# Optimization experiments

Hardware: AMD Instinct MI355X
Metric: run time of the kernel (lower is better)

The kernel has to match this reference:

```python
import jax, jax.numpy as jnp
import numpy as np

N_NODES = 50000
N_EDGES = 600000
N_GRAPHS = 256
N_FL1, N_MPL, N_FL2, N_FL3 = 128, 128, 128, 64
EPS = 1e-12


def _glorot(key, shape):
    lim = float(np.sqrt(6.0 / (shape[0] + shape[1])))
    return jax.random.uniform(key, shape, jnp.float32, -lim, lim)


def setup_inputs() -> dict:
    key = jax.random.key(0)
    ks = jax.random.split(key, 16)
    x = jax.random.normal(ks[0], (N_NODES, 5), jnp.float32)
    edge_index = jax.random.randint(ks[1], (2, N_EDGES), 0, N_NODES, jnp.int64)
    batch = jnp.sort(jax.random.randint(ks[2], (N_NODES,), 0, N_GRAPHS, jnp.int64))
    return {
        "x": x,
        "edge_index": edge_index,
        "batch": batch,
        "W_pre": _glorot(ks[3], (5, N_FL1)),
        "b_pre": jnp.zeros((N_FL1,), jnp.float32),
        "W1_l": _glorot(ks[4], (N_FL1, N_MPL)),
        "b1": jnp.zeros((N_MPL,), jnp.float32),
        "W1_r": _glorot(ks[5], (N_FL1, N_MPL)),
        "W2_l": _glorot(ks[6], (N_MPL, N_MPL)),
        "b2": jnp.zeros((N_MPL,), jnp.float32),
        "W2_r": _glorot(ks[7], (N_MPL, N_MPL)),
        "W_p1": _glorot(ks[8], (N_MPL, N_FL2)),
        "b_p1": jnp.zeros((N_FL2,), jnp.float32),
        "W_p2": _glorot(ks[9], (N_FL2, N_FL3)),
        "b_p2": jnp.zeros((N_FL3,), jnp.float32),
        "W_out": _glorot(ks[10], (N_FL3, 1)),
        "b_out": jnp.zeros((1,), jnp.float32),
    }


def _sage_conv(x, src, dst, deg_inv, W_l, b_l, W_r):
    # mean-aggregate neighbor messages x[src] onto dst, then linear transforms
    agg = jax.ops.segment_sum(x[src], dst, num_segments=N_NODES) * deg_inv  # [N, d]
    out = agg @ W_l + b_l + x @ W_r
    # normalize=True -> L2 normalize per node (PyG F.normalize, eps=1e-12)
    norm = jnp.sqrt(jnp.sum(out * out, axis=-1, keepdims=True))
    return out / jnp.maximum(norm, EPS)


def reference(x, edge_index, batch, W_pre, b_pre, W1_l, b1, W1_r,
              W2_l, b2, W2_r, W_p1, b_p1, W_p2, b_p2, W_out, b_out):
    src, dst = edge_index[0], edge_index[1]
    deg = jax.ops.segment_sum(jnp.ones((N_EDGES,), jnp.float32), dst, num_segments=N_NODES)
    deg_inv = (1.0 / jnp.maximum(deg, 1.0))[:, None]

    h = jax.nn.relu(x @ W_pre + b_pre)
    h = jax.nn.relu(_sage_conv(h, src, dst, deg_inv, W1_l, b1, W1_r))
    h = jax.nn.relu(_sage_conv(h, src, dst, deg_inv, W2_l, b2, W2_r))

    # global_mean_pool over graph ids in batch
    g_sum = jax.ops.segment_sum(h, batch, num_segments=N_GRAPHS)  # [G, d]
    g_cnt = jax.ops.segment_sum(jnp.ones((N_NODES,), jnp.float32), batch, num_segments=N_GRAPHS)
    g = g_sum / jnp.maximum(g_cnt, 1.0)[:, None]

    g = jax.nn.relu(g @ W_p1 + b_p1)
    g = jax.nn.relu(g @ W_p2 + b_p2)
    return g @ W_out + b_out  # [G, 1]
```

## Files before the change

### kernel.cpp

```cpp
#include <hip/hip_runtime.h>
#include <hip/hip_bf16.h>

#define N_NODES 50000
#define N_EDGES 600000
#define N_GRAPHS 256
#define D 128
#define NTILES 1563

typedef __bf16 bf16x8 __attribute__((ext_vector_type(8)));
typedef float f32x16 __attribute__((ext_vector_type(16)));
typedef unsigned short u16x8 __attribute__((ext_vector_type(8)));
typedef unsigned short u16x4 __attribute__((ext_vector_type(4)));

__device__ __forceinline__ float bf2f(unsigned short u) {
    unsigned v = ((unsigned)u) << 16;
    return __builtin_bit_cast(float, v);
}
__device__ __forceinline__ unsigned short f2bf(float f) {
    unsigned x = __builtin_bit_cast(unsigned, f);
    unsigned r = (x + 0x7fffu + ((x >> 16) & 1u)) >> 16;
    return (unsigned short)r;
}


__global__ void zero_int_kernel(int* __restrict__ p, int n) {
    int i = blockIdx.x * 256 + threadIdx.x;
    if (i < n) p[i] = 0;
}

__global__ void deg_kernel(const int* __restrict__ dst, int* __restrict__ deg) {
    int e = blockIdx.x * 256 + threadIdx.x;
    if (e < N_EDGES) atomicAdd(&deg[dst[e]], 1);
}

__global__ __launch_bounds__(1024) void scan_blk_kernel(const int* __restrict__ deg,
                                                        int* __restrict__ partial,
                                                        int* __restrict__ bsum) {
    __shared__ int tmp[1024];
    int tid = threadIdx.x;
    int i = blockIdx.x * 1024 + tid;
    int v = (i < N_NODES) ? deg[i] : 0;
    tmp[tid] = v;
    __syncthreads();
    for (int off = 1; off < 1024; off <<= 1) {
        int add = (tid >= off) ? tmp[tid - off] : 0;
        __syncthreads();
        tmp[tid] += add;
        __syncthreads();
    }
    if (i < N_NODES) partial[i] = tmp[tid] - v;
    if (tid == 1023) bsum[blockIdx.x] = tmp[tid];
}

__global__ void scan_top_kernel(const int* __restrict__ bsum, int* __restrict__ boff,
                                int* __restrict__ row_start, int nblk) {
    int l = threadIdx.x;
    int v = (l < nblk) ? bsum[l] : 0;
    int incl = v;
#pragma unroll
    for (int m = 1; m < 64; m <<= 1) {
        int t = __shfl_up(incl, m);
        if (l >= m) incl += t;
    }
    if (l < nblk) boff[l] = incl - v;
    if (l == 63) row_start[N_NODES] = incl;
}

__global__ void scan_fix_kernel(const int* __restrict__ partial, const int* __restrict__ boff,
                                const int* __restrict__ deg, int* __restrict__ row_start,
                                int* __restrict__ cursor, float* __restrict__ deg_inv) {
    int i = blockIdx.x * 256 + threadIdx.x;
    if (i >= N_NODES) return;
    int rs = partial[i] + boff[i >> 10];
    row_start[i] = rs;
    cursor[i] = rs;
    deg_inv[i] = 1.0f / fmaxf((float)deg[i], 1.0f);
}

__global__ void fill_kernel(const int* __restrict__ src, const int* __restrict__ dst,
                            int* __restrict__ cursor, int* __restrict__ csr_src) {
    int e = blockIdx.x * 256 + threadIdx.x;
    if (e < N_EDGES) {
        int slot = atomicAdd(&cursor[dst[e]], 1);
        csr_src[slot] = src[e];
    }
}


__global__ void pack_w_kernel(const float* __restrict__ Wl1, const float* __restrict__ Wr1,
                              const float* __restrict__ Wl2, const float* __restrict__ Wr2,
                              unsigned short* __restrict__ Wp) {
    int tid = blockIdx.x * 256 + threadIdx.x;
    int conv = tid >> 15;
    int e = tid & 32767;
    int j = e & 7, lane = (e >> 3) & 63, ct = (e >> 9) & 3, kt = e >> 11;
    int k = kt * 16 + (lane >> 5) * 8 + j;
    int col = (lane & 31) * 4 + ct;
    const float* Wl = conv ? Wl2 : Wl1;
    const float* Wr = conv ? Wr2 : Wr1;
    float v = (k < 128) ? Wl[k * 128 + col] : Wr[(k - 128) * 128 + col];
    Wp[tid] = f2bf(v);
}


__global__ void pre_kernel(const float* __restrict__ x, const float* __restrict__ Wp,
                           const float* __restrict__ bp, unsigned short* __restrict__ h0) {
    int idx = blockIdx.x * 256 + threadIdx.x;
    if (idx >= N_NODES * 16) return;
    int node = idx >> 4, j8 = (idx & 15) * 8;
    const float* xr = x + node * 5;
    float acc[8];
#pragma unroll
    for (int c = 0; c < 8; ++c) acc[c] = bp[j8 + c];
#pragma unroll
    for (int k = 0; k < 5; ++k) {
        float xv = xr[k];
#pragma unroll
        for (int c = 0; c < 8; ++c) acc[c] += xv * Wp[k * D + j8 + c];
    }
    u16x8 o;
#pragma unroll
    for (int c = 0; c < 8; ++c) o[c] = f2bf(fmaxf(acc[c], 0.f));
    *(u16x8*)&h0[(size_t)node * D + j8] = o;
}


__global__ __launch_bounds__(256) void agg_kernel(const unsigned short* __restrict__ h,
                                                  const int* __restrict__ row_start,
                                                  const int* __restrict__ csr_src,
                                                  const float* __restrict__ deg_inv,
                                                  unsigned short* __restrict__ aggb) {
    int node = blockIdx.x * 16 + (threadIdx.x >> 4);
    int fl = threadIdx.x & 15;
    if (node >= N_NODES) return;
    int s = row_start[node], e = row_start[node + 1];
    float a[8] = {0.f, 0.f, 0.f, 0.f, 0.f, 0.f, 0.f, 0.f};
    int i = s;
    for (; i + 3 < e; i += 4) {
        int c0 = csr_src[i];
        int c1 = csr_src[i + 1];
        int c2 = csr_src[i + 2];
        int c3 = csr_src[i + 3];
        bf16x8 v0 = *(const bf16x8*)(h + (size_t)c0 * D + fl * 8);
        bf16x8 v1 = *(const bf16x8*)(h + (size_t)c1 * D + fl * 8);
        bf16x8 v2 = *(const bf16x8*)(h + (size_t)c2 * D + fl * 8);
        bf16x8 v3 = *(const bf16x8*)(h + (size_t)c3 * D + fl * 8);
#pragma unroll
        for (int j = 0; j < 8; ++j)
            a[j] += ((float)v0[j] + (float)v1[j]) + ((float)v2[j] + (float)v3[j]);
    }
    for (; i < e; ++i) {
        int c0 = csr_src[i];
        bf16x8 v0 = *(const bf16x8*)(h + (size_t)c0 * D + fl * 8);
#pragma unroll
        for (int j = 0; j < 8; ++j) a[j] += (float)v0[j];
    }
    float di = deg_inv[node];
    u16x8 o;
#pragma unroll
    for (int j = 0; j < 8; ++j) o[j] = f2bf(a[j] * di);
    *(u16x8*)(aggb + (size_t)node * D + fl * 8) = o;
}


__global__ __launch_bounds__(256) void lin_mfma_kernel(const unsigned short* __restrict__ hin,
                                                       const unsigned short* __restrict__ aggb,
                                                       const unsigned short* __restrict__ Wp,
                                                       const float* __restrict__ b,
                                                       unsigned short* __restrict__ hout) {
    int wg = blockIdx.x * 4 + (threadIdx.x >> 6);
    if (wg >= NTILES) return;
    int lane = threadIdx.x & 63;
    int l31 = lane & 31, hi = lane >> 5;
    int row0 = wg * 32;
    int rowg = row0 + l31;
    if (rowg > N_NODES - 1) rowg = N_NODES - 1;

    const unsigned short* arow = aggb + (size_t)rowg * D + hi * 8;
    const unsigned short* hrow = hin + (size_t)rowg * D + hi * 8;
    const unsigned short* wbase = Wp + lane * 8;

    f32x16 acc[4];
#pragma unroll
    for (int ct = 0; ct < 4; ++ct) acc[ct] = (f32x16)(0.0f);

#pragma unroll
    for (int kt = 0; kt < 16; ++kt) {
        const unsigned short* asrc = (kt < 8) ? (arow + kt * 16) : (hrow + (kt - 8) * 16);
        bf16x8 af = *(const bf16x8*)asrc;
#pragma unroll
        for (int ct = 0; ct < 4; ++ct) {
            bf16x8 bfrag = *(const bf16x8*)(wbase + (kt * 4 + ct) * 512);
            acc[ct] = __builtin_amdgcn_mfma_f32_32x32x16_bf16(af, bfrag, acc[ct], 0, 0, 0);
        }
    }

    float4 b4 = *(const float4*)&b[l31 * 4];
    float bb[4] = {b4.x, b4.y, b4.z, b4.w};

#pragma unroll
    for (int r = 0; r < 16; ++r) {
        float v[4];
        float ss = 0.f;
#pragma unroll
        for (int ct = 0; ct < 4; ++ct) {
            v[ct] = acc[ct][r] + bb[ct];
            ss += v[ct] * v[ct];
        }
        ss += __shfl_xor(ss, 1);
        ss += __shfl_xor(ss, 2);
        ss += __shfl_xor(ss, 4);
        ss += __shfl_xor(ss, 8);
        ss += __shfl_xor(ss, 16);
        float sc = 1.0f / fmaxf(sqrtf(ss), 1e-12f);
        int row = row0 + (r & 3) + 8 * (r >> 2) + 4 * hi;
        if (row < N_NODES) {
            u16x4 o;
#pragma unroll
            for (int ct = 0; ct < 4; ++ct) o[ct] = f2bf(fmaxf(v[ct] * sc, 0.f));
            *(u16x4*)(hout + (size_t)row * D + l31 * 4) = o;
        }
    }
}


__global__ __launch_bounds__(128) void pool_sum_kernel(const unsigned short* __restrict__ h,
                                                       const int* __restrict__ batch,
                                                       float* __restrict__ gsum) {
    int j = threadIdx.x;
    int i0 = blockIdx.x * 128;
    int i1 = i0 + 128;
    if (i1 > N_NODES) i1 = N_NODES;
    __shared__ int bids[128];
    if (i0 + j < N_NODES) bids[j] = batch[i0 + j];
    __syncthreads();
    float acc = 0.f;
    int cur = bids[0];
    for (int i = i0; i < i1; ++i) {
        int bid = bids[i - i0];
        if (bid != cur) {
            atomicAdd(&gsum[cur * D + j], acc);
            acc = 0.f;
            cur = bid;
        }
        acc += bf2f(h[(size_t)i * D + j]);
    }
    atomicAdd(&gsum[cur * D + j], acc);
}


__global__ __launch_bounds__(128) void mlp_kernel(const float* __restrict__ gsum,
                                                  const int* __restrict__ batch,
                                                  const float* __restrict__ Wp1,
                                                  const float* __restrict__ bp1,
                                                  const float* __restrict__ Wp2,
                                                  const float* __restrict__ bp2,
                                                  const float* __restrict__ Wout,
                                                  const float* __restrict__ bout,
                                                  float* __restrict__ out) {
    __shared__ float gin[128], y1[128], y2[64];
    __shared__ float cnt_s;
    int gid = blockIdx.x, j = threadIdx.x;
    if (j == 0) {
        int lo = 0, hi = N_NODES;
        while (lo < hi) { int m = (lo + hi) >> 1; if (batch[m] < gid) lo = m + 1; else hi = m; }
        int start = lo;
        lo = start; hi = N_NODES;
        while (lo < hi) { int m = (lo + hi) >> 1; if (batch[m] < gid + 1) lo = m + 1; else hi = m; }
        cnt_s = fmaxf((float)(lo - start), 1.0f);
    }
    __syncthreads();
    gin[j] = gsum[gid * 128 + j] / cnt_s;
    __syncthreads();
    float a = bp1[j];
    for (int k = 0; k < 128; ++k) a += gin[k] * Wp1[k * 128 + j];
    y1[j] = fmaxf(a, 0.f);
    __syncthreads();
    if (j < 64) {
        float a2 = bp2[j];
        for (int k = 0; k < 128; ++k) a2 += y1[k] * Wp2[k * 64 + j];
        y2[j] = fmaxf(a2, 0.f);
    }
    __syncthreads();
    if (j < 64) {
        float v = y2[j] * Wout[j];
#pragma unroll
        for (int m = 32; m >= 1; m >>= 1) v += __shfl_xor(v, m);
        if (j == 0) out[gid] = v + bout[0];
    }
}


extern "C" void kernel_launch(void* const* d_in, const int* in_sizes, int n_in,
                              void* d_out, int out_size, void* d_ws, size_t ws_size,
                              hipStream_t stream) {
    const float* x     = (const float*)d_in[0];
    const int*   ei    = (const int*)d_in[1];
    const int*   batch = (const int*)d_in[2];
    const float* W_pre = (const float*)d_in[3];
    const float* b_pre = (const float*)d_in[4];
    const float* W1_l  = (const float*)d_in[5];
    const float* b1    = (const float*)d_in[6];
    const float* W1_r  = (const float*)d_in[7];
    const float* W2_l  = (const float*)d_in[8];
    const float* b2    = (const float*)d_in[9];
    const float* W2_r  = (const float*)d_in[10];
    const float* W_p1  = (const float*)d_in[11];
    const float* b_p1  = (const float*)d_in[12];
    const float* W_p2  = (const float*)d_in[13];
    const float* b_p2  = (const float*)d_in[14];
    const float* W_out = (const float*)d_in[15];
    const float* b_out = (const float*)d_in[16];

    const int* src = ei;
    const int* dst = ei + N_EDGES;

    size_t off = 0;
    auto carve = [&](size_t bytes) {
        void* p = (char*)d_ws + off;
        off += (bytes + 255) & ~(size_t)255;
        return p;
    };
    int* deg       = (int*)carve(50048 * 4 + 32768 * 4);
    float* gsum    = (float*)(deg + 50048);
    int* row_start = (int*)carve((N_NODES + 1) * 4);
    int* cursor    = (int*)carve(N_NODES * 4);
    int* csr_src   = (int*)carve(N_EDGES * 4);
    float* deg_inv = (float*)carve(N_NODES * 4);
    int* partial   = (int*)carve(N_NODES * 4);
    int* bsum      = (int*)carve(64 * 4);
    int* boff      = (int*)carve(64 * 4);
    unsigned short* h0   = (unsigned short*)carve((size_t)N_NODES * D * 2);
    unsigned short* h1   = (unsigned short*)carve((size_t)N_NODES * D * 2);
    unsigned short* aggb = (unsigned short*)carve((size_t)N_NODES * D * 2);
    unsigned short* Wp   = (unsigned short*)carve(65536 * 2);
    unsigned short* h2 = h0;
    float* out = (float*)d_out;

    const int nblk_scan = (N_NODES + 1023) / 1024;

    pack_w_kernel<<<256, 256, 0, stream>>>(W1_l, W1_r, W2_l, W2_r, Wp);

    zero_int_kernel<<<(50048 + 32768 + 255) / 256, 256, 0, stream>>>(deg, 50048 + 32768);
    deg_kernel<<<(N_EDGES + 255) / 256, 256, 0, stream>>>(dst, deg);
    scan_blk_kernel<<<nblk_scan, 1024, 0, stream>>>(deg, partial, bsum);
    scan_top_kernel<<<1, 64, 0, stream>>>(bsum, boff, row_start, nblk_scan);
    scan_fix_kernel<<<(N_NODES + 255) / 256, 256, 0, stream>>>(partial, boff, deg,
                                                               row_start, cursor, deg_inv);
    fill_kernel<<<(N_EDGES + 255) / 256, 256, 0, stream>>>(src, dst, cursor, csr_src);

    pre_kernel<<<(N_NODES * 16 + 255) / 256, 256, 0, stream>>>(x, W_pre, b_pre, h0);

    agg_kernel<<<(N_NODES + 15) / 16, 256, 0, stream>>>(h0, row_start, csr_src, deg_inv, aggb);
    lin_mfma_kernel<<<(NTILES + 3) / 4, 256, 0, stream>>>(h0, aggb, Wp, b1, h1);

    agg_kernel<<<(N_NODES + 15) / 16, 256, 0, stream>>>(h1, row_start, csr_src, deg_inv, aggb);
    lin_mfma_kernel<<<(NTILES + 3) / 4, 256, 0, stream>>>(h1, aggb, Wp + 32768, b2, h2);

    pool_sum_kernel<<<(N_NODES + 127) / 128, 128, 0, stream>>>(h2, batch, gsum);
    mlp_kernel<<<N_GRAPHS, 128, 0, stream>>>(gsum, batch, W_p1, b_p1, W_p2, b_p2,
                                             W_out, b_out, out);
}
```

Baseline: 215.3 us.

## Fuse neighbor aggregation into MFMA conv kernel and merge init kernels

Gathers and mean-aggregates neighbor rows directly into MFMA A-fragments inside the linear kernel, so the intermediate aggb buffer and its separate kernel pass disappear. Zeroing, weight packing and the pre-layer are merged into one multi-role launch. The scan's top-level pass is folded into scan_fix, where each block sums the preceding block totals itself. The fused conv kernel assigns one lane per node with a 64-float accumulator and 16 outstanding 16-byte loads per edge pair. That raises register pressure and leaves few lanes per node doing the gather, which may hurt memory parallelism and occupancy compared with the old 16-lanes-per-node gather.

Measured after the change: 229.9 us. 6.8% more time.

```diff
diff --git a/kernel.cpp b/kernel.cpp
--- a/kernel.cpp
+++ b/kernel.cpp
@@ -23,10 +23,54 @@
 }
 
 
-__global__ void zero_int_kernel(int* __restrict__ p, int n) {
-    int i = blockIdx.x * 256 + threadIdx.x;
-    if (i < n) p[i] = 0;
-}
+#define ZERO_N (50048 + 32768)
+#define ZERO_BLOCKS 324
+#define PACK_BLOCKS 256
+#define PRE_BLOCKS 3125
+
+__global__ __launch_bounds__(256) void init_kernel(
+    int* __restrict__ deg_gsum,
+    const float* __restrict__ Wl1, const float* __restrict__ Wr1,
+    const float* __restrict__ Wl2, const float* __restrict__ Wr2,
+    unsigned short* __restrict__ Wpk,
+    const float* __restrict__ x, const float* __restrict__ Wpre,
+    const float* __restrict__ bpre, unsigned short* __restrict__ h0) {
+    int bb = blockIdx.x;
+    if (bb < ZERO_BLOCKS) {
+        int i = bb * 256 + threadIdx.x;
+        if (i < ZERO_N) deg_gsum[i] = 0;
+    } else if (bb < ZERO_BLOCKS + PACK_BLOCKS) {
+        int tid = (bb - ZERO_BLOCKS) * 256 + threadIdx.x;
+        int conv = tid >> 15;
+        int e = tid & 32767;
+        int j = e & 7, lane = (e >> 3) & 63, ct = (e >> 9) & 3, kt = e >> 11;
+        int k = kt * 16 + (lane >> 5) * 8 + j;
+        int col = (lane & 31) * 4 + ct;
+        const float* Wl = conv ? Wl2 : Wl1;
+        const float* Wr = conv ? Wr2 : Wr1;
+        float v = (k < 128) ? Wl[k * 128 + col] : Wr[(k - 128) * 128 + col];
+        Wpk[tid] = f2bf(v);
+    } else {
+        int idx = (bb - ZERO_BLOCKS - PACK_BLOCKS) * 256 + threadIdx.x;
+        if (idx >= N_NODES * 16) return;
+        int node = idx >> 4, j8 = (idx & 15) * 8;
+        const float* xr = x + node * 5;
+        float acc[8];
+#pragma unroll
+        for (int c = 0; c < 8; ++c) acc[c] = bpre[j8 + c];
+#pragma unroll
+        for (int k = 0; k < 5; ++k) {
+            float xv = xr[k];
+#pragma unroll
+            for (int c = 0; c < 8; ++c) acc[c] += xv * Wpre[k * D + j8 + c];
+        }
+        u16x8 o;
+#pragma unroll
+        for (int c = 0; c < 8; ++c) o[c] = f2bf(fmaxf(acc[c], 0.f));
+        *(u16x8*)&h0[(size_t)node * D + j8] = o;
+    }
+}
+
 
 __global__ void deg_kernel(const int* __restrict__ dst, int* __restrict__ deg) {
     int e = blockIdx.x * 256 + threadIdx.x;
@@ -52,29 +96,30 @@
     if (tid == 1023) bsum[blockIdx.x] = tmp[tid];
 }
 
-__global__ void scan_top_kernel(const int* __restrict__ bsum, int* __restrict__ boff,
-                                int* __restrict__ row_start, int nblk) {
-    int l = threadIdx.x;
-    int v = (l < nblk) ? bsum[l] : 0;
-    int incl = v;
-#pragma unroll
-    for (int m = 1; m < 64; m <<= 1) {
-        int t = __shfl_up(incl, m);
-        if (l >= m) incl += t;
-    }
-    if (l < nblk) boff[l] = incl - v;
-    if (l == 63) row_start[N_NODES] = incl;
-}
-
-__global__ void scan_fix_kernel(const int* __restrict__ partial, const int* __restrict__ boff,
-                                const int* __restrict__ deg, int* __restrict__ row_start,
-                                int* __restrict__ cursor, float* __restrict__ deg_inv) {
+__global__ __launch_bounds__(256) void scan_fix_kernel(const int* __restrict__ partial,
+                                                       const int* __restrict__ bsum,
+                                                       const int* __restrict__ deg,
+                                                       int* __restrict__ row_start,
+                                                       int* __restrict__ cursor,
+                                                       float* __restrict__ deg_inv) {
+    __shared__ int boff_s;
+    int bucket = (blockIdx.x * 256) >> 10;
+    if (threadIdx.x < 64) {
+        int l = threadIdx.x;
+        int v = (l < bucket) ? bsum[l] : 0;
+#pragma unroll
+        for (int m = 32; m >= 1; m >>= 1) v += __shfl_xor(v, m);
+        if (l == 0) boff_s = v;
+    }
+    __syncthreads();
     int i = blockIdx.x * 256 + threadIdx.x;
     if (i >= N_NODES) return;
-    int rs = partial[i] + boff[i >> 10];
+    int dg = deg[i];
+    int rs = partial[i] + boff_s;
     row_start[i] = rs;
     cursor[i] = rs;
-    deg_inv[i] = 1.0f / fmaxf((float)deg[i], 1.0f);
+    deg_inv[i] = 1.0f / fmaxf((float)dg, 1.0f);
+    if (i == N_NODES - 1) row_start[N_NODES] = rs + dg;
 }
 
 __global__ void fill_kernel(const int* __restrict__ src, const int* __restrict__ dst,
@@ -87,117 +132,87 @@
 }
 
 
-__global__ void pack_w_kernel(const float* __restrict__ Wl1, const float* __restrict__ Wr1,
-                              const float* __restrict__ Wl2, const float* __restrict__ Wr2,
-                              unsigned short* __restrict__ Wp) {
-    int tid = blockIdx.x * 256 + threadIdx.x;
-    int conv = tid >> 15;
-    int e = tid & 32767;
-    int j = e & 7, lane = (e >> 3) & 63, ct = (e >> 9) & 3, kt = e >> 11;
-    int k = kt * 16 + (lane >> 5) * 8 + j;
-    int col = (lane & 31) * 4 + ct;
-    const float* Wl = conv ? Wl2 : Wl1;
-    const float* Wr = conv ? Wr2 : Wr1;
-    float v = (k < 128) ? Wl[k * 128 + col] : Wr[(k - 128) * 128 + col];
-    Wp[tid] = f2bf(v);
-}
-
-
-__global__ void pre_kernel(const float* __restrict__ x, const float* __restrict__ Wp,
-                           const float* __restrict__ bp, unsigned short* __restrict__ h0) {
-    int idx = blockIdx.x * 256 + threadIdx.x;
-    if (idx >= N_NODES * 16) return;
-    int node = idx >> 4, j8 = (idx & 15) * 8;
-    const float* xr = x + node * 5;
-    float acc[8];
-#pragma unroll
-    for (int c = 0; c < 8; ++c) acc[c] = bp[j8 + c];
-#pragma unroll
-    for (int k = 0; k < 5; ++k) {
-        float xv = xr[k];
-#pragma unroll
-        for (int c = 0; c < 8; ++c) acc[c] += xv * Wp[k * D + j8 + c];
-    }
-    u16x8 o;
-#pragma unroll
-    for (int c = 0; c < 8; ++c) o[c] = f2bf(fmaxf(acc[c], 0.f));
-    *(u16x8*)&h0[(size_t)node * D + j8] = o;
-}
-
-
-__global__ __launch_bounds__(256) void agg_kernel(const unsigned short* __restrict__ h,
-                                                  const int* __restrict__ row_start,
-                                                  const int* __restrict__ csr_src,
-                                                  const float* __restrict__ deg_inv,
-                                                  unsigned short* __restrict__ aggb) {
-    int node = blockIdx.x * 16 + (threadIdx.x >> 4);
-    int fl = threadIdx.x & 15;
-    if (node >= N_NODES) return;
-    int s = row_start[node], e = row_start[node + 1];
-    float a[8] = {0.f, 0.f, 0.f, 0.f, 0.f, 0.f, 0.f, 0.f};
-    int i = s;
-    for (; i + 3 < e; i += 4) {
-        int c0 = csr_src[i];
-        int c1 = csr_src[i + 1];
-        int c2 = csr_src[i + 2];
-        int c3 = csr_src[i + 3];
-        bf16x8 v0 = *(const bf16x8*)(h + (size_t)c0 * D + fl * 8);
-        bf16x8 v1 = *(const bf16x8*)(h + (size_t)c1 * D + fl * 8);
-        bf16x8 v2 = *(const bf16x8*)(h + (size_t)c2 * D + fl * 8);
-        bf16x8 v3 = *(const bf16x8*)(h + (size_t)c3 * D + fl * 8);
-#pragma unroll
-        for (int j = 0; j < 8; ++j)
-            a[j] += ((float)v0[j] + (float)v1[j]) + ((float)v2[j] + (float)v3[j]);
-    }
-    for (; i < e; ++i) {
-        int c0 = csr_src[i];
-        bf16x8 v0 = *(const bf16x8*)(h + (size_t)c0 * D + fl * 8);
-#pragma unroll
-        for (int j = 0; j < 8; ++j) a[j] += (float)v0[j];
-    }
-    float di = deg_inv[node];
-    u16x8 o;
-#pragma unroll
-    for (int j = 0; j < 8; ++j) o[j] = f2bf(a[j] * di);
-    *(u16x8*)(aggb + (size_t)node * D + fl * 8) = o;
-}
-
-
-__global__ __launch_bounds__(256) void lin_mfma_kernel(const unsigned short* __restrict__ hin,
-                                                       const unsigned short* __restrict__ aggb,
-                                                       const unsigned short* __restrict__ Wp,
-                                                       const float* __restrict__ b,
-                                                       unsigned short* __restrict__ hout) {
+__global__ __launch_bounds__(256) void conv_kernel(const unsigned short* __restrict__ hin,
+                                                   const int* __restrict__ row_start,
+                                                   const int* __restrict__ csr_src,
+                                                   const float* __restrict__ deg_inv,
+                                                   const unsigned short* __restrict__ Wp,
+                                                   const float* __restrict__ b,
+                                                   unsigned short* __restrict__ hout) {
     int wg = blockIdx.x * 4 + (threadIdx.x >> 6);
     if (wg >= NTILES) return;
     int lane = threadIdx.x & 63;
     int l31 = lane & 31, hi = lane >> 5;
     int row0 = wg * 32;
     int rowg = row0 + l31;
-    if (rowg > N_NODES - 1) rowg = N_NODES - 1;
-
-    const unsigned short* arow = aggb + (size_t)rowg * D + hi * 8;
-    const unsigned short* hrow = hin + (size_t)rowg * D + hi * 8;
+    bool valid = rowg < N_NODES;
+    int rowc = valid ? rowg : (N_NODES - 1);
+
+    int s = valid ? row_start[rowg] : 0;
+    int e = valid ? row_start[rowg + 1] : 0;
+    float di = valid ? deg_inv[rowg] : 1.0f;
+
+    float a[8][8];
+#pragma unroll
+    for (int kt = 0; kt < 8; ++kt)
+#pragma unroll
+        for (int j = 0; j < 8; ++j) a[kt][j] = 0.f;
+
+    int i = s;
+    for (; i + 1 < e; i += 2) {
+        int c0 = csr_src[i];
+        int c1 = csr_src[i + 1];
+        const unsigned short* p0 = hin + (size_t)c0 * D + hi * 8;
+        const unsigned short* p1 = hin + (size_t)c1 * D + hi * 8;
+        bf16x8 v0[8], v1[8];
+#pragma unroll
+        for (int kt = 0; kt < 8; ++kt) {
+            v0[kt] = *(const bf16x8*)(p0 + kt * 16);
+            v1[kt] = *(const bf16x8*)(p1 + kt * 16);
+        }
+#pragma unroll
+        for (int kt = 0; kt < 8; ++kt)
+#pragma unroll
+            for (int j = 0; j < 8; ++j) a[kt][j] += (float)v0[kt][j] + (float)v1[kt][j];
+    }
+    if (i < e) {
+        int c0 = csr_src[i];
+        const unsigned short* p0 = hin + (size_t)c0 * D + hi * 8;
+#pragma unroll
+        for (int kt = 0; kt < 8; ++kt) {
+            bf16x8 v0 = *(const bf16x8*)(p0 + kt * 16);
+#pragma unroll
+            for (int j = 0; j < 8; ++j) a[kt][j] += (float)v0[j];
+        }
+    }
+
+    bf16x8 afr[16];
+#pragma unroll
+    for (int kt = 0; kt < 8; ++kt) {
+        u16x8 t;
+#pragma unroll
+        for (int j = 0; j < 8; ++j) t[j] = f2bf(a[kt][j] * di);
+        afr[kt] = __builtin_bit_cast(bf16x8, t);
+    }
+    const unsigned short* hrow = hin + (size_t)rowc * D + hi * 8;
+#pragma unroll
+    for (int kt = 0; kt < 8; ++kt) afr[8 + kt] = *(const bf16x8*)(hrow + kt * 16);
+
     const unsigned short* wbase = Wp + lane * 8;
-
     f32x16 acc[4];
 #pragma unroll
     for (int ct = 0; ct < 4; ++ct) acc[ct] = (f32x16)(0.0f);
-
 #pragma unroll
     for (int kt = 0; kt < 16; ++kt) {
-        const unsigned short* asrc = (kt < 8) ? (arow + kt * 16) : (hrow + (kt - 8) * 16);
-        bf16x8 af = *(const bf16x8*)asrc;
 #pragma unroll
         for (int ct = 0; ct < 4; ++ct) {
             bf16x8 bfrag = *(const bf16x8*)(wbase + (kt * 4 + ct) * 512);
-            acc[ct] = __builtin_amdgcn_mfma_f32_32x32x16_bf16(af, bfrag, acc[ct], 0, 0, 0);
+            acc[ct] = __builtin_amdgcn_mfma_f32_32x32x16_bf16(afr[kt], bfrag, acc[ct], 0, 0, 0);
         }
     }
 
     float4 b4 = *(const float4*)&b[l31 * 4];
     float bb[4] = {b4.x, b4.y, b4.z, b4.w};
-
 #pragma unroll
     for (int r = 0; r < 16; ++r) {
         float v[4];
@@ -329,33 +344,27 @@
     float* deg_inv = (float*)carve(N_NODES * 4);
     int* partial   = (int*)carve(N_NODES * 4);
     int* bsum      = (int*)carve(64 * 4);
-    int* boff      = (int*)carve(64 * 4);
-    unsigned short* h0   = (unsigned short*)carve((size_t)N_NODES * D * 2);
-    unsigned short* h1   = (unsigned short*)carve((size_t)N_NODES * D * 2);
-    unsigned short* aggb = (unsigned short*)carve((size_t)N_NODES * D * 2);
-    unsigned short* Wp   = (unsigned short*)carve(65536 * 2);
+    unsigned short* h0 = (unsigned short*)carve((size_t)N_NODES * D * 2);
+    unsigned short* h1 = (unsigned short*)carve((size_t)N_NODES * D * 2);
+    unsigned short* Wp = (unsigned short*)carve(65536 * 2);
     unsigned short* h2 = h0;
     float* out = (float*)d_out;
 
     const int nblk_scan = (N_NODES + 1023) / 1024;
 
-    pack_w_kernel<<<256, 256, 0, stream>>>(W1_l, W1_r, W2_l, W2_r, Wp);
-
-    zero_int_kernel<<<(50048 + 32768 + 255) / 256, 256, 0, stream>>>(deg, 50048 + 32768);
+    init_kernel<<<ZERO_BLOCKS + PACK_BLOCKS + PRE_BLOCKS, 256, 0, stream>>>(
+        deg, W1_l, W1_r, W2_l, W2_r, Wp, x, W_pre, b_pre, h0);
+
     deg_kernel<<<(N_EDGES + 255) / 256, 256, 0, stream>>>(dst, deg);
     scan_blk_kernel<<<nblk_scan, 1024, 0, stream>>>(deg, partial, bsum);
-    scan_top_kernel<<<1, 64, 0, stream>>>(bsum, boff, row_start, nblk_scan);
-    scan_fix_kernel<<<(N_NODES + 255) / 256, 256, 0, stream>>>(partial, boff, deg,
+    scan_fix_kernel<<<(N_NODES + 255) / 256, 256, 0, stream>>>(partial, bsum, deg,
                                                                row_start, cursor, deg_inv);
     fill_kernel<<<(N_EDGES + 255) / 256, 256, 0, stream>>>(src, dst, cursor, csr_src);
 
-    pre_kernel<<<(N_NODES * 16 + 255) / 256, 256, 0, stream>>>(x, W_pre, b_pre, h0);
-
-    agg_kernel<<<(N_NODES + 15) / 16, 256, 0, stream>>>(h0, row_start, csr_src, deg_inv, aggb);
-    lin_mfma_kernel<<<(NTILES + 3) / 4, 256, 0, stream>>>(h0, aggb, Wp, b1, h1);
-
-    agg_kernel<<<(N_NODES + 15) / 16, 256, 0, stream>>>(h1, row_start, csr_src, deg_inv, aggb);
-    lin_mfma_kernel<<<(NTILES + 3) / 4, 256, 0, stream>>>(h1, aggb, Wp + 32768, b2, h2);
+    conv_kernel<<<(NTILES + 3) / 4, 256, 0, stream>>>(h0, row_start, csr_src, deg_inv,
+                                                      Wp, b1, h1);
+    conv_kernel<<<(NTILES + 3) / 4, 256, 0, stream>>>(h1, row_start, csr_src, deg_inv,
+                                                      Wp + 32768, b2, h2);
 
     pool_sum_kernel<<<(N_NODES + 127) / 128, 128, 0, stream>>>(h2, batch, gsum);
     mlp_kernel<<<N_GRAPHS, 128, 0, stream>>>(gsum, batch, W_p1, b_p1, W_p2, b_p2,
```
